# Kernel optimization log

Measured on AMD Instinct MI355X. Metric: run time of the kernel, lower is better.

Reference implementation:

```python
import jax, jax.numpy as jnp
import numpy as np

T, B, H, EMB, EVO, A = 700, 32, 800, 32, 21, 60
DIN = EMB + EVO            # 53 = embedding + evolutionary profile
RNN_OUT = 2 * H + DIN      # 1653 = bi-LSTM output + skip connection

BOND_LENGTHS = jnp.array([145.801, 152.326, 132.868], jnp.float32)
BOND_ANGLES = jnp.array([2.124, 1.941, 2.028], jnp.float32)
INIT_MAT = jnp.array([[-np.sqrt(0.5), np.sqrt(1.5), 0.0],
                      [-np.sqrt(2.0), 0.0, 0.0],
                      [0.0, 0.0, 0.0]], jnp.float32)


def setup_inputs():
    key = jax.random.key(0)
    ks = jax.random.split(key, 12)
    s = 0.03  # ~ pytorch LSTM uniform(-1/sqrt(H), 1/sqrt(H)) scale

    def lstm_params(k, d):
        k1, k2, k3 = jax.random.split(k, 3)
        return (jax.random.normal(k1, (4 * H, d)) * s,
                jax.random.normal(k2, (4 * H, H)) * s,
                jax.random.normal(k3, (4 * H,)) * s)  # b = b_ih + b_hh fused

    Wih0f, Whh0f, b0f = lstm_params(ks[0], DIN)
    Wih0b, Whh0b, b0b = lstm_params(ks[1], DIN)
    Wih1f, Whh1f, b1f = lstm_params(ks[2], 2 * H)
    Wih1b, Whh1b, b1b = lstm_params(ks[3], 2 * H)
    emb = jax.random.normal(ks[4], (21, EMB)) * s
    emb = emb.at[0].set(0.0)  # padding_idx=0
    fcW = jax.random.normal(ks[5], (A, RNN_OUT)) * s
    fcb = jax.random.normal(ks[6], (A,)) * s
    alphabet = jnp.pi * jnp.tanh(jax.random.normal(ks[7], (A, 3)))  # angularize
    primary = jax.random.randint(ks[8], (T, B), 0, 21)
    evolutionary = jax.random.normal(ks[9], (T, B, EVO))
    return {"primary": primary, "evolutionary": evolutionary, "seq_length": T,
            "emb": emb,
            "Wih0f": Wih0f, "Whh0f": Whh0f, "b0f": b0f,
            "Wih0b": Wih0b, "Whh0b": Whh0b, "b0b": b0b,
            "Wih1f": Wih1f, "Whh1f": Whh1f, "b1f": b1f,
            "Wih1b": Wih1b, "Whh1b": Whh1b, "b1b": b1b,
            "fcW": fcW, "fcb": fcb, "alphabet": alphabet}


def lstm_dir(xs, Wih, Whh, b, reverse):
    """One direction of an LSTM over xs [T, B, D] -> [T, B, H] (PyTorch gate order i,f,g,o)."""
    if reverse:
        xs = xs[::-1]
    xg = jnp.einsum('tbd,gd->tbg', xs, Wih) + b  # precompute input projection

    def step(carry, g_t):
        h, c = carry
        g = g_t + h @ Whh.T
        i, f, gg, o = jnp.split(g, 4, axis=-1)
        c = jax.nn.sigmoid(f) * c + jax.nn.sigmoid(i) * jnp.tanh(gg)
        h = jax.nn.sigmoid(o) * jnp.tanh(c)
        return (h, c), h

    z = jnp.zeros((xs.shape[1], Whh.shape[1]), xs.dtype)
    _, hs = jax.lax.scan(step, (z, z), xg)
    return hs[::-1] if reverse else hs


def dihedral_to_point(dih):
    """dih [T, B, 3] -> backbone points in local frames [3T, B, 3]."""
    rct = BOND_LENGTHS * jnp.cos(jnp.pi - BOND_ANGLES)
    rst = BOND_LENGTHS * jnp.sin(jnp.pi - BOND_ANGLES)
    px = jnp.broadcast_to(rct, dih.shape)
    pts = jnp.stack([px, jnp.cos(dih) * rst, jnp.sin(dih) * rst], axis=-1)  # [T,B,3,3]
    t, b = dih.shape[0], dih.shape[1]
    return pts.transpose(0, 2, 1, 3).reshape(3 * t, b, 3)


def point_to_coordinate(pts):
    """Sequential NeRF extension: pts [3T, B, 3] -> coords [3T, B, 3]."""
    b_sz = pts.shape[1]
    a = jnp.broadcast_to(INIT_MAT[0], (b_sz, 3))
    b = jnp.broadcast_to(INIT_MAT[1], (b_sz, 3))
    c = jnp.broadcast_to(INIT_MAT[2], (b_sz, 3))

    def norm(v):
        return v / jnp.sqrt(jnp.sum(v * v, axis=-1, keepdims=True) + 1e-12)

    def step(carry, p):
        a, b, c = carry
        bc = norm(c - b)
        n = norm(jnp.cross(b - a, bc))
        coord = c + p[:, 0:1] * bc + p[:, 1:2] * jnp.cross(n, bc) + p[:, 2:3] * n
        return (b, c, coord), coord

    _, coords = jax.lax.scan(step, (a, b, c), pts)
    return coords


def reference(primary, evolutionary, seq_length, emb,
              Wih0f, Whh0f, b0f, Wih0b, Whh0b, b0b,
              Wih1f, Whh1f, b1f, Wih1b, Whh1b, b1b,
              fcW, fcb, alphabet):
    # seq_length == T for all sequences, so packing is identity.
    x = jnp.concatenate([emb[primary], evolutionary], axis=-1)  # [T,B,53]
    h0 = jnp.concatenate([lstm_dir(x, Wih0f, Whh0f, b0f, False),
                          lstm_dir(x, Wih0b, Whh0b, b0b, True)], axis=-1)   # [T,B,1600]
    h1 = jnp.concatenate([lstm_dir(h0, Wih1f, Whh1f, b1f, False),
                          lstm_dir(h0, Wih1b, Whh1b, b1b, True)], axis=-1)  # [T,B,1600]
    out = jnp.concatenate([h1, x], axis=-1)  # skip connection -> [T,B,1653]
    logits = jnp.einsum('tbd,ad->tba', out, fcW) + fcb  # [T,B,60]
    probs = jax.nn.softmax(logits, axis=-1)  # alphabet_temperature = 1.0
    dih = jnp.arctan2(probs @ jnp.sin(alphabet), probs @ jnp.cos(alphabet))  # [T,B,3]
    return point_to_coordinate(dihedral_to_point(dih))  # [3T, B, 3]
```

## Files before the change

### kernel.cpp

```cpp
#include <hip/hip_runtime.h>
#include <hip/hip_bf16.h>
#include <math.h>


typedef unsigned int u32;
typedef unsigned long long u64;
typedef __bf16 bf16x8 __attribute__((ext_vector_type(8)));
typedef float  f32x4  __attribute__((ext_vector_type(4)));

#define TT 700
#define BT 32
#define HROW 1664
#define CH 50
#define NCH (TT / CH)
#define SLOT ((size_t)2 * CH * 3200 * 32)
#define LDS_L0 (108 * 512 + 102400)
#define LDS_L1 (100 * 512 + 102400)

__device__ __forceinline__ f32x4 mfma16(bf16x8 a, bf16x8 b, f32x4 c) {
  return __builtin_amdgcn_mfma_f32_16x16x32_bf16(a, b, c, 0, 0, 0);
}
__device__ __forceinline__ float sigf(float x) { return 1.f / (1.f + __expf(-x)); }

#define ALOAD(p)    __hip_atomic_load((p), __ATOMIC_RELAXED, __HIP_MEMORY_SCOPE_AGENT)
#define ASTORE(p,v) __hip_atomic_store((p), (v), __ATOMIC_RELAXED, __HIP_MEMORY_SCOPE_AGENT)

__device__ __forceinline__ void lds_barrier() {
  asm volatile("s_waitcnt lgkmcnt(0)" ::: "memory");
  __builtin_amdgcn_s_barrier();
}

__device__ __forceinline__ bf16x8 cvt8(f32x4 a, f32x4 b) {
  bf16x8 r;
  r[0] = (__bf16)a[0]; r[1] = (__bf16)a[1]; r[2] = (__bf16)a[2]; r[3] = (__bf16)a[3];
  r[4] = (__bf16)b[0]; r[5] = (__bf16)b[1]; r[6] = (__bf16)b[2]; r[7] = (__bf16)b[3];
  return r;
}

#define QUAD_TRANSPOSE(l_, a0, a1, a2, a3, o0, o1, o2, o3)                   \
  {                                                                          \
    float s0 = __shfl_xor(a0, 1), s1 = __shfl_xor(a1, 1);                    \
    float s2 = __shfl_xor(a2, 1), s3 = __shfl_xor(a3, 1);                    \
    const bool e1 = ((l_) & 1) == 0;                                         \
    float n0 = e1 ? a0 : s1, n1 = e1 ? s0 : a1;                              \
    float n2 = e1 ? a2 : s3, n3 = e1 ? s2 : a3;                              \
    float t0 = __shfl_xor(n0, 2), t1 = __shfl_xor(n1, 2);                    \
    float t2 = __shfl_xor(n2, 2), t3 = __shfl_xor(n3, 2);                    \
    const bool e2 = ((l_) & 2) == 0;                                         \
    o0 = e2 ? n0 : t2; o1 = e2 ? n1 : t3;                                    \
    o2 = e2 ? t0 : n2; o3 = e2 ? t1 : n3;                                    \
  }

__global__ void pack_wx0_kernel(const float* Wih0f, const float* Wih0b, __bf16* wx0) {
  int idx = blockIdx.x * 256 + threadIdx.x;
  if (idx >= 2 * 3200 * 64) return;
  int d = idx / (3200 * 64);
  int r = (idx / 64) % 3200;
  int k = idx % 64;
  const float* W = d ? Wih0b : Wih0f;
  wx0[idx] = (k < 53) ? (__bf16)W[(size_t)r * 53 + k] : (__bf16)0.f;
}

__global__ void pack_fc_kernel(const float* fcW, __bf16* wfc) {
  int idx = blockIdx.x * 256 + threadIdx.x;
  if (idx >= 64 * 1664) return;
  int a = idx / 1664, k = idx % 1664;
  __bf16 v = (__bf16)0.f;
  if (a < 60 && k < 1653) v = (__bf16)fcW[(size_t)a * 1653 + k];
  wfc[idx] = v;
}

__global__ void xpad_kernel(const int* primary, const float* evo,
                            const float* emb, __bf16* xpad) {
  int idx = blockIdx.x * 256 + threadIdx.x;
  int t = idx >> 11;
  int b = (idx >> 6) & 31;
  int k = idx & 63;
  __bf16 v = (__bf16)0.f;
  if (k < 32)      v = (__bf16)emb[primary[t * 32 + b] * 32 + k];
  else if (k < 53) v = (__bf16)evo[((size_t)t * 32 + b) * 21 + (k - 32)];
  xpad[idx] = v;
}

__global__ void small_init_kernel(__bf16* zerobuf, u32* flags,
                                  float* sinA, float* cosA, const float* alpha) {
  int idx = blockIdx.x * 256 + threadIdx.x;
  if (idx < 32 * HROW) zerobuf[idx] = (__bf16)0.f;
  if (idx < 11392) flags[idx] = 0u;
  int j = idx - 32 * HROW;
  if (j >= 0 && j < 192) {
    if (j < 180) {
      float v = alpha[j];
      sinA[j] = sinf(v);
      cosA[j] = cosf(v);
    } else { sinA[j] = 0.f; cosA[j] = 0.f; }
  }
}

__device__ __forceinline__ void wait_lines(u32* flags, int base, int count,
                                           unsigned gen) {
  const int tid = threadIdx.x;
  if (tid < 64) {
    int spin = 0;
    for (;;) {
      bool ok = true;
      for (int j = tid; j < count; j += 64)
        ok = ok && (ALOAD(flags + (size_t)(base + j) * 32) >= gen);
      if (__popcll(__ballot(ok)) == 64) break;
      if (++spin > 24) __builtin_amdgcn_s_sleep(1);
    }
  }
  __syncthreads();
}

__device__ __forceinline__ void rec_barrier(u32* flags, unsigned gen,
                                            int base, int count) {
  asm volatile("s_waitcnt vmcnt(0)" ::: "memory");
  __syncthreads();
  if (threadIdx.x == 0) ASTORE(flags + (size_t)blockIdx.x * 32, gen);
  wait_lines(flags, base, count, gen);
}

struct L0Args {
  const __bf16 *xpad, *wx0, *zero;
  const float *Whh0f, *Whh0b, *b0f, *b0b;
  __bf16* h0;
  u32* flags;
};

__global__ __launch_bounds__(256, 1) void lstm_l0(L0Args A) {
  extern __shared__ __bf16 u2[];
  const int wg = blockIdx.x, d = wg / 50, u0 = (wg % 50) * 16;
  const int tid = threadIdx.x, w = tid >> 6, l = tid & 63;
  const int nidx = l & 15, q = l >> 4, bL = l & 31, gl = l >> 5;
  const int dcol = d * 832;
  const int row = (nidx & 3) * 800 + u0 + 4 * w + (nidx >> 2);
  const float bias_n = (d ? A.b0b : A.b0f)[row];
  const float* wrf = (d ? A.Whh0b : A.Whh0f) + (size_t)row * 800 + q * 8;
  __bf16* wlds = u2 + 108 * 256;

#pragma unroll
  for (int sl = 0; sl < 25; ++sl) {
    f32x4 wa = *(const f32x4*)(wrf + sl * 32);
    f32x4 wb = *(const f32x4*)(wrf + sl * 32 + 4);
    *(bf16x8*)(wlds + ((size_t)(w * 25 + sl) * 64 + l) * 8) = cvt8(wa, wb);
  }
  const __bf16* wx_row = A.wx0 + (size_t)d * 3200 * 64 + (size_t)row * 64 + q * 8;
  bf16x8 wx_r0 = *(const bf16x8*)wx_row;
  bf16x8 wx_r1 = *(const bf16x8*)(wx_row + 32);
  __syncthreads();

  float cA = 0.f, cB = 0.f;
#pragma unroll 1
  for (int s = 0; s < TT; ++s) {
    const int tt = d ? (TT - 1 - s) : s;
    const __bf16* hprev =
        (s == 0) ? A.zero : (A.h0 + (size_t)(d ? tt + 1 : tt - 1) * (BT * HROW));

    bf16x8 hreg[13];
    const __bf16* hsrc = hprev + (size_t)bL * HROW + dcol;
#pragma unroll
    for (int i = 0; i < 12; ++i)
      hreg[i] = *(const bf16x8*)(hsrc + (i * 8 + w * 2 + gl) * 8);
    if (w < 2) hreg[12] = *(const bf16x8*)(hsrc + (96 + w * 2 + gl) * 8);
    bf16x8 xv = *(const bf16x8*)(A.xpad + ((size_t)tt * BT + bL) * 64 + (tid >> 5) * 8);

#pragma unroll
    for (int i = 0; i < 12; ++i)
      *(bf16x8*)(u2 + (size_t)(i * 8 + w * 2 + gl) * 256 + bL * 8) = hreg[i];
    if (w < 2)
      *(bf16x8*)(u2 + (size_t)(96 + w * 2 + gl) * 256 + bL * 8) = hreg[12];
    *(bf16x8*)(u2 + (size_t)(100 + (tid >> 5)) * 256 + bL * 8) = xv;
    __syncthreads();

    f32x4 acc0 = {0.f, 0.f, 0.f, 0.f}, acc1 = {0.f, 0.f, 0.f, 0.f};
#pragma unroll
    for (int sl = 0; sl < 27; ++sl) {
      bf16x8 bfr;
      if (sl < 25)
        bfr = *(const bf16x8*)(wlds + ((size_t)(w * 25 + sl) * 64 + l) * 8);
      else
        bfr = (sl == 25) ? wx_r0 : wx_r1;
      const __bf16* ab = u2 + (size_t)(sl * 4 + q) * 256 + nidx * 8;
      bf16x8 a0 = *(const bf16x8*)ab;
      bf16x8 a1 = *(const bf16x8*)(ab + 128);
      acc0 = mfma16(a0, bfr, acc0);
      acc1 = mfma16(a1, bfr, acc1);
    }

    {
      float a0 = acc0[0] + bias_n, a1 = acc0[1] + bias_n,
            a2 = acc0[2] + bias_n, a3 = acc0[3] + bias_n;
      float e0 = acc1[0] + bias_n, e1v = acc1[1] + bias_n,
            e2v = acc1[2] + bias_n, e3 = acc1[3] + bias_n;
      float iA, fA, gA, oA, iB, fB, gB, oB;
      QUAD_TRANSPOSE(l, a0, a1, a2, a3, iA, fA, gA, oA);
      QUAD_TRANSPOSE(l, e0, e1v, e2v, e3, iB, fB, gB, oB);
      cA = sigf(fA) * cA + sigf(iA) * tanhf(gA);
      float hA = sigf(oA) * tanhf(cA);
      cB = sigf(fB) * cB + sigf(iB) * tanhf(gB);
      float hB = sigf(oB) * tanhf(cB);
      float hA2 = __shfl_xor(hA, 4);
      float hB2 = __shfl_xor(hB, 4);
      if ((l & 4) == 0) {
        const int bA = q * 4 + (nidx & 3);
        const int colp = dcol + u0 + 4 * w + (nidx >> 2);
        union { u32 u; __bf16 h2[2]; } pk;
        pk.h2[0] = (__bf16)hA; pk.h2[1] = (__bf16)hA2;
        ASTORE((u32*)(A.h0 + ((size_t)tt * BT + bA) * HROW + colp), pk.u);
        pk.h2[0] = (__bf16)hB; pk.h2[1] = (__bf16)hB2;
        ASTORE((u32*)(A.h0 + ((size_t)tt * BT + bA + 16) * HROW + colp), pk.u);
      }
    }

    if (s < TT - 1) rec_barrier(A.flags, (unsigned)(s + 1), d * 50, 50);
  }
}

struct L1Args {
  const __bf16 *h0, *zero;
  const float *Whh1f, *Whh1b, *Wih1f, *Wih1b, *b1f, *b1b;
  __bf16 *h1, *xg;
  u32* flags;
};

__global__ __launch_bounds__(256, 1) void lstm_l1(L1Args A) {
  extern __shared__ __bf16 u2[];
  const int tid = threadIdx.x, w = tid >> 6, l = tid & 63;
  const int nidx = l & 15, q = l >> 4, bL = l & 31, gl = l >> 5;
  __bf16* wlds = u2 + 100 * 256;

  if (blockIdx.x < 100) {
    const int wg = blockIdx.x, d = wg / 50, u0 = (wg % 50) * 16;
    const int dcol = d * 832;
    const int row = (nidx & 3) * 800 + u0 + 4 * w + (nidx >> 2);
    {
      const float* wrf = (d ? A.Whh1b : A.Whh1f) + (size_t)row * 800 + q * 8;
#pragma unroll
      for (int sl = 0; sl < 25; ++sl) {
        f32x4 wa = *(const f32x4*)(wrf + sl * 32);
        f32x4 wb = *(const f32x4*)(wrf + sl * 32 + 4);
        *(bf16x8*)(wlds + ((size_t)(w * 25 + sl) * 64 + l) * 8) = cvt8(wa, wb);
      }
    }
    __syncthreads();
    float cA = 0.f, cB = 0.f;

    for (int k = 0; k < NCH; ++k) {
      wait_lines(A.flags, 100, 156, (unsigned)(k + 1));
      const __bf16* buf = A.xg + (size_t)(k & 1) * SLOT;
      const u64* xga0 = (const u64*)(buf + ((size_t)(d * CH) * 3200 + row) * 32 + q * 4);
      u64 x0 = ALOAD(xga0);
      u64 x1 = ALOAD(xga0 + 4);
#pragma unroll 1
      for (int si = 0; si < CH; ++si) {
        const int s = k * CH + si;
        const int tt = d ? (TT - 1 - s) : s;
        const __bf16* hprev =
            (s == 0) ? A.zero
                     : (A.h1 + (size_t)(d ? tt + 1 : tt - 1) * (BT * HROW));

        u64 cx0 = x0, cx1 = x1;
        if (si + 1 < CH) {
          const u64* xgn = (const u64*)(buf +
              ((size_t)(d * CH + si + 1) * 3200 + row) * 32 + q * 4);
          x0 = ALOAD(xgn);
          x1 = ALOAD(xgn + 4);
        }

        bf16x8 hreg[13];
        const __bf16* hsrc = hprev + (size_t)bL * HROW + dcol;
#pragma unroll
        for (int i = 0; i < 12; ++i)
          hreg[i] = *(const bf16x8*)(hsrc + (i * 8 + w * 2 + gl) * 8);
        if (w < 2) hreg[12] = *(const bf16x8*)(hsrc + (96 + w * 2 + gl) * 8);

        union { u64 u; __bf16 h[4]; } ux0, ux1;
        ux0.u = cx0; ux1.u = cx1;
        f32x4 acc0 = {(float)ux0.h[0], (float)ux0.h[1],
                      (float)ux0.h[2], (float)ux0.h[3]};
        f32x4 acc1 = {(float)ux1.h[0], (float)ux1.h[1],
                      (float)ux1.h[2], (float)ux1.h[3]};

#pragma unroll
        for (int i = 0; i < 12; ++i)
          *(bf16x8*)(u2 + (size_t)(i * 8 + w * 2 + gl) * 256 + bL * 8) = hreg[i];
        if (w < 2)
          *(bf16x8*)(u2 + (size_t)(96 + w * 2 + gl) * 256 + bL * 8) = hreg[12];
        lds_barrier();

#pragma unroll
        for (int sl = 0; sl < 25; ++sl) {
          bf16x8 bfr = *(const bf16x8*)(wlds + ((size_t)(w * 25 + sl) * 64 + l) * 8);
          const __bf16* ab = u2 + (size_t)(sl * 4 + q) * 256 + nidx * 8;
          bf16x8 a0 = *(const bf16x8*)ab;
          bf16x8 a1 = *(const bf16x8*)(ab + 128);
          acc0 = mfma16(a0, bfr, acc0);
          acc1 = mfma16(a1, bfr, acc1);
        }

        {
          float a0 = acc0[0], a1 = acc0[1], a2 = acc0[2], a3 = acc0[3];
          float e0 = acc1[0], e1v = acc1[1], e2v = acc1[2], e3 = acc1[3];
          float iA, fA, gA, oA, iB, fB, gB, oB;
          QUAD_TRANSPOSE(l, a0, a1, a2, a3, iA, fA, gA, oA);
          QUAD_TRANSPOSE(l, e0, e1v, e2v, e3, iB, fB, gB, oB);
          cA = sigf(fA) * cA + sigf(iA) * tanhf(gA);
          float hA = sigf(oA) * tanhf(cA);
          cB = sigf(fB) * cB + sigf(iB) * tanhf(gB);
          float hB = sigf(oB) * tanhf(cB);
          float hA2 = __shfl_xor(hA, 4);
          float hB2 = __shfl_xor(hB, 4);
          if ((l & 4) == 0) {
            const int bA = q * 4 + (nidx & 3);
            const int colp = dcol + u0 + 4 * w + (nidx >> 2);
            union { u32 u; __bf16 h2[2]; } pk;
            pk.h2[0] = (__bf16)hA; pk.h2[1] = (__bf16)hA2;
            ASTORE((u32*)(A.h1 + ((size_t)tt * BT + bA) * HROW + colp), pk.u);
            pk.h2[0] = (__bf16)hB; pk.h2[1] = (__bf16)hB2;
            ASTORE((u32*)(A.h1 + ((size_t)tt * BT + bA + 16) * HROW + colp), pk.u);
          }
        }

        if (s < TT - 1) rec_barrier(A.flags, (unsigned)(s + 1), 0 + d * 50, 50);
      }
    }
  } else {
    const int g = blockIdx.x - 100;
    const int u_begin = (g * 400) / 156;
    const int u_end   = ((g + 1) * 400) / 156;
    const int nslots  = (u_end - u_begin) * 50;
    const int rh = w >> 1, bh = w & 1;

    bf16x8 pre[13];
    f32x4 acc = {0.f, 0.f, 0.f, 0.f};
    int cur_tl = -1;
    float bn = 0.f;
    int rr = 0;

    for (int k = 0; k < NCH; ++k) {
      if (k >= 2) wait_lines(A.flags, 0, 100, (unsigned)((k - 1) * CH));
      __bf16* buf = A.xg + (size_t)(k & 1) * SLOT;

      {
        const int th0 = u_begin & 1;
        const int dir0 = (u_begin >> 1) / 100;
        const int tloc0 = th0 * 25;
        const int t0 = dir0 ? (TT - 1 - k * CH - tloc0) : (k * CH + tloc0);
        const __bf16* hs = A.h0 + ((size_t)t0 * BT + bL) * HROW;
#pragma unroll
        for (int i = 0; i < 12; ++i)
          pre[i] = *(const bf16x8*)(hs + (i * 8 + w * 2 + gl) * 8);
        if (w < 2) pre[12] = *(const bf16x8*)(hs + (96 + w * 2 + gl) * 8);
      }

#pragma unroll 1
      for (int s = 0; s < nslots; ++s) {
        const int u = u_begin + s / 50;
        const int r = s % 50;
        const int tl = u >> 1, th = u & 1;
        const int tloc = th * 25 + (r >> 1);
        const int pass = r & 1;
        const int dir = tl / 100, rt = tl % 100;
        const int rbase = rt * 32;

        if (tl != cur_tl) {
          cur_tl = tl;
          const float* W = dir ? A.Wih1b : A.Wih1f;
          __syncthreads();
          for (int i = w * 25; i < w * 25 + 25; ++i) {
            const int rhh = i / 50, sl = i % 50;
            const int rrr = rbase + rhh * 16 + nidx;
            const float* wp = W + (size_t)rrr * 1600 + sl * 32 + q * 8;
            f32x4 wa = *(const f32x4*)wp;
            f32x4 wb = *(const f32x4*)(wp + 4);
            *(bf16x8*)(wlds + ((size_t)i * 64 + l) * 8) = cvt8(wa, wb);
          }
          __syncthreads();
          rr = rbase + rh * 16 + nidx;
          bn = (dir ? A.b1b : A.b1f)[rr];
        }

#pragma unroll
        for (int i = 0; i < 12; ++i)
          *(bf16x8*)(u2 + (size_t)(i * 8 + w * 2 + gl) * 256 + bL * 8) = pre[i];
        if (w < 2)
          *(bf16x8*)(u2 + (size_t)(96 + w * 2 + gl) * 256 + bL * 8) = pre[12];
        lds_barrier();

        if (s + 1 < nslots) {
          const int s2 = s + 1;
          const int un = u_begin + s2 / 50;
          const int r2 = s2 % 50;
          const int thn = un & 1;
          const int tlocn = thn * 25 + (r2 >> 1);
          const int passn = r2 & 1;
          const int dirn = (un >> 1) / 100;
          const int tn = dirn ? (TT - 1 - k * CH - tlocn) : (k * CH + tlocn);
          const __bf16* hs = A.h0 + ((size_t)tn * BT + bL) * HROW + passn * 832;
#pragma unroll
          for (int i = 0; i < 12; ++i)
            pre[i] = *(const bf16x8*)(hs + (i * 8 + w * 2 + gl) * 8);
          if (w < 2) pre[12] = *(const bf16x8*)(hs + (96 + w * 2 + gl) * 8);
        }
        __builtin_amdgcn_sched_barrier(0);

        if (pass == 0) acc = f32x4{0.f, 0.f, 0.f, 0.f};
#pragma unroll
        for (int sl = 0; sl < 25; ++sl) {
          bf16x8 b = *(const bf16x8*)(wlds +
              ((size_t)(rh * 50 + pass * 25 + sl) * 64 + l) * 8);
          bf16x8 a = *(const bf16x8*)(u2 +
              (size_t)(sl * 4 + q) * 256 + (bh * 16 + nidx) * 8);
          acc = mfma16(a, b, acc);
        }
        lds_barrier();

        if (pass == 1) {
          union { u64 u; __bf16 h[4]; } pv;
#pragma unroll
          for (int r2 = 0; r2 < 4; ++r2) pv.h[r2] = (__bf16)(acc[r2] + bn);
          ASTORE((u64*)(buf + ((size_t)(dir * CH + tloc) * 3200 + rr) * 32 +
                        bh * 16 + q * 4), pv.u);
        }
      }
      asm volatile("s_waitcnt vmcnt(0)" ::: "memory");
      __syncthreads();
      if (tid == 0) ASTORE(A.flags + (size_t)(100 + g) * 32, (unsigned)(k + 1));
    }
  }
}

__global__ __launch_bounds__(256) void fc_kernel(
    const __bf16* __restrict__ h1, const __bf16* __restrict__ xpad,
    const __bf16* __restrict__ wfc, const float* __restrict__ fcb,
    const float* __restrict__ sinA, const float* __restrict__ cosA,
    float* __restrict__ pts) {
  __shared__ float lg[32 * 64];
  const int t = blockIdx.x, tid = threadIdx.x;
  const int wave = tid >> 6, lane = tid & 63, nidx = lane & 15, q = lane >> 4;
  const int a_col = wave * 16 + nidx;
  const __bf16* wrow = wfc + (size_t)a_col * 1664 + q * 8;
  const __bf16* h1row = h1 + (size_t)t * BT * HROW;
  const __bf16* xrow  = xpad + (size_t)t * BT * 64;
  f32x4 acc0 = {0.f, 0.f, 0.f, 0.f}, acc1 = {0.f, 0.f, 0.f, 0.f};
#pragma unroll
  for (int sl = 0; sl < 52; ++sl) {
    const int k = sl * 32 + q * 8;
    bf16x8 a0, a1;
    if (sl < 50) {
      const int kp = (sl < 25) ? k : (k + 32);
      a0 = *(const bf16x8*)(h1row + (size_t)nidx * HROW + kp);
      a1 = *(const bf16x8*)(h1row + (size_t)(16 + nidx) * HROW + kp);
    } else {
      a0 = *(const bf16x8*)(xrow + nidx * 64 + (k - 1600));
      a1 = *(const bf16x8*)(xrow + (16 + nidx) * 64 + (k - 1600));
    }
    bf16x8 bfr = *(const bf16x8*)(wrow + sl * 32);
    acc0 = mfma16(a0, bfr, acc0);
    acc1 = mfma16(a1, bfr, acc1);
  }
  const float bn = (a_col < 60) ? fcb[a_col] : -1e30f;
#pragma unroll
  for (int r = 0; r < 4; ++r) {
    lg[(q * 4 + r) * 64 + a_col]      = acc0[r] + bn;
    lg[(16 + q * 4 + r) * 64 + a_col] = acc1[r] + bn;
  }
  __syncthreads();

  const int b = tid >> 3, j = tid & 7;
  float v[8];
  float m = -1e30f;
#pragma unroll
  for (int k2 = 0; k2 < 8; ++k2) {
    v[k2] = lg[b * 64 + j + 8 * k2];
    m = fmaxf(m, v[k2]);
  }
  m = fmaxf(m, __shfl_xor(m, 1, 8));
  m = fmaxf(m, __shfl_xor(m, 2, 8));
  m = fmaxf(m, __shfl_xor(m, 4, 8));
  float s = 0.f;
#pragma unroll
  for (int k2 = 0; k2 < 8; ++k2) { v[k2] = __expf(v[k2] - m); s += v[k2]; }
  s += __shfl_xor(s, 1, 8);
  s += __shfl_xor(s, 2, 8);
  s += __shfl_xor(s, 4, 8);
  const float inv = 1.f / s;
  float ps[3] = {0.f, 0.f, 0.f}, pc[3] = {0.f, 0.f, 0.f};
#pragma unroll
  for (int k2 = 0; k2 < 8; ++k2) {
    const int a = j + 8 * k2;
    const float p = v[k2] * inv;
#pragma unroll
    for (int c = 0; c < 3; ++c) {
      ps[c] += p * sinA[a * 3 + c];
      pc[c] += p * cosA[a * 3 + c];
    }
  }
#pragma unroll
  for (int c = 0; c < 3; ++c) {
    ps[c] += __shfl_xor(ps[c], 1, 8);
    ps[c] += __shfl_xor(ps[c], 2, 8);
    ps[c] += __shfl_xor(ps[c], 4, 8);
    pc[c] += __shfl_xor(pc[c], 1, 8);
    pc[c] += __shfl_xor(pc[c], 2, 8);
    pc[c] += __shfl_xor(pc[c], 4, 8);
  }
  if (j == 0) {
    const float BL[3] = {145.801f, 152.326f, 132.868f};
    const float BA[3] = {2.124f, 1.941f, 2.028f};
#pragma unroll
    for (int c = 0; c < 3; ++c) {
      const float ang = 3.14159265358979323846f - BA[c];
      const float rct = BL[c] * cosf(ang), rst = BL[c] * sinf(ang);
      const float dih = atan2f(ps[c], pc[c]);
      float* o = pts + ((size_t)(3 * t + c) * BT + b) * 3;
      o[0] = rct;
      o[1] = cosf(dih) * rst;
      o[2] = sinf(dih) * rst;
    }
  }
}

__global__ void nerf_kernel(const float* __restrict__ pts, float* __restrict__ out) {
  const int b = threadIdx.x;
  if (b >= 32) return;
  float ax = -0.70710678f, ay = 1.22474487f, az = 0.f;
  float bx = -1.41421356f, by = 0.f, bz = 0.f;
  float cx = 0.f, cy = 0.f, cz = 0.f;
#pragma unroll 4
  for (int i = 0; i < 3 * TT; ++i) {
    const float* p = pts + ((size_t)i * BT + b) * 3;
    const float p0 = p[0], p1 = p[1], p2 = p[2];
    float ux = cx - bx, uy = cy - by, uz = cz - bz;
    const float ri = rsqrtf(ux * ux + uy * uy + uz * uz + 1e-12f);
    ux *= ri; uy *= ri; uz *= ri;
    const float wx = bx - ax, wy = by - ay, wz = bz - az;
    float nx = wy * uz - wz * uy, ny = wz * ux - wx * uz, nz = wx * uy - wy * ux;
    const float rn = rsqrtf(nx * nx + ny * ny + nz * nz + 1e-12f);
    nx *= rn; ny *= rn; nz *= rn;
    const float mx = ny * uz - nz * uy, my = nz * ux - nx * uz, mz = nx * uy - ny * ux;
    const float ox = cx + p0 * ux + p1 * mx + p2 * nx;
    const float oy = cy + p0 * uy + p1 * my + p2 * ny;
    const float oz = cz + p0 * uz + p1 * mz + p2 * nz;
    out[((size_t)i * BT + b) * 3 + 0] = ox;
    out[((size_t)i * BT + b) * 3 + 1] = oy;
    out[((size_t)i * BT + b) * 3 + 2] = oz;
    ax = bx; ay = by; az = bz;
    bx = cx; by = cy; bz = cz;
    cx = ox; cy = oy; cz = oz;
  }
}

extern "C" void kernel_launch(void* const* d_in, const int* in_sizes, int n_in,
                              void* d_out, int out_size, void* d_ws, size_t ws_size,
                              hipStream_t stream) {
  (void)in_sizes; (void)n_in; (void)out_size;
  const int*   primary = (const int*)d_in[0];
  const float* evo     = (const float*)d_in[1];
  const float* emb     = (const float*)d_in[3];
  const float* Wih0f   = (const float*)d_in[4];
  const float* Whh0f   = (const float*)d_in[5];
  const float* b0f     = (const float*)d_in[6];
  const float* Wih0b   = (const float*)d_in[7];
  const float* Whh0b   = (const float*)d_in[8];
  const float* b0b     = (const float*)d_in[9];
  const float* Wih1f   = (const float*)d_in[10];
  const float* Whh1f   = (const float*)d_in[11];
  const float* b1f     = (const float*)d_in[12];
  const float* Wih1b   = (const float*)d_in[13];
  const float* Whh1b   = (const float*)d_in[14];
  const float* b1b     = (const float*)d_in[15];
  const float* fcW     = (const float*)d_in[16];
  const float* fcb     = (const float*)d_in[17];
  const float* alpha   = (const float*)d_in[18];

  char* ws = (char*)d_ws;
  size_t off = 0;
  auto take = [&](size_t n) -> void* {
    void* p = ws + off;
    off += (n + 511) & ~(size_t)511;
    return p;
  };
  __bf16* xpad = (__bf16*)take((size_t)TT * BT * 64 * 2);
  __bf16* zb   = (__bf16*)take((size_t)BT * HROW * 2);
  __bf16* wx0  = (__bf16*)take((size_t)2 * 3200 * 64 * 2);
  __bf16* wfc  = (__bf16*)take((size_t)64 * 1664 * 2);
  float*  sinA = (float*)take(192 * 4);
  float*  cosA = (float*)take(192 * 4);
  float*  pts  = (float*)take((size_t)3 * TT * BT * 3 * 4);
  u32*    flags0 = (u32*)take(11392 * 4);
  u32*    flags1 = flags0 + 3200;
  __bf16* xg   = (__bf16*)take(2 * SLOT * 2);
  __bf16* h0   = (__bf16*)take((size_t)TT * BT * HROW * 2);
  __bf16* h1   = (__bf16*)take((size_t)TT * BT * HROW * 2);
  if (off > ws_size) return;

  static int lds_cfg = 0;
  if (!lds_cfg) {
    hipFuncSetAttribute((const void*)lstm_l0,
                        hipFuncAttributeMaxDynamicSharedMemorySize, LDS_L0);
    hipFuncSetAttribute((const void*)lstm_l1,
                        hipFuncAttributeMaxDynamicSharedMemorySize, LDS_L1);
    lds_cfg = 1;
  }

  pack_wx0_kernel<<<1600, 256, 0, stream>>>(Wih0f, Wih0b, wx0);
  pack_fc_kernel<<<(64 * 1664 + 255) / 256, 256, 0, stream>>>(fcW, wfc);
  xpad_kernel<<<(TT * BT * 64) / 256, 256, 0, stream>>>(primary, evo, emb, xpad);
  small_init_kernel<<<209, 256, 0, stream>>>(zb, flags0, sinA, cosA, alpha);

  L0Args a0;
  a0.xpad = xpad; a0.wx0 = wx0; a0.zero = zb;
  a0.Whh0f = Whh0f; a0.Whh0b = Whh0b; a0.b0f = b0f; a0.b0b = b0b;
  a0.h0 = h0; a0.flags = flags0;
  lstm_l0<<<100, 256, LDS_L0, stream>>>(a0);

  L1Args a1;
  a1.h0 = h0; a1.zero = zb;
  a1.Whh1f = Whh1f; a1.Whh1b = Whh1b;
  a1.Wih1f = Wih1f; a1.Wih1b = Wih1b;
  a1.b1f = b1f; a1.b1b = b1b;
  a1.h1 = h1; a1.xg = xg; a1.flags = flags1;
  lstm_l1<<<256, 256, LDS_L1, stream>>>(a1);

  fc_kernel<<<TT, 256, 0, stream>>>(h1, xpad, wfc, fcb, sinA, cosA, pts);
  nerf_kernel<<<1, 64, 0, stream>>>(pts, (float*)d_out);
}
```

Before: 9.200 ms.

## Fuse both LSTM layers into one persistent kernel overlapping layer-1 input projection

Merges the layer-0 and layer-1 recurrent kernels into a single persistent launch. Recurrent blocks run layer 0 and then layer 1, while the 156 helper blocks compute layer-1 input projections chunk by chunk as soon as the needed layer-0 timesteps from both directions are ready. The helpers follow a reordered chunk schedule with six xg buffer slots, so layer-1 can start on its first chunks without waiting for all of layer 0. This is meant to hide the input-projection GEMM and the launch gap behind the layer-0 recurrence. It costs more workspace and adds complex flag-based cross-block dependencies, falling back to two slots in sequential order if the workspace is too small.

```diff
diff --git a/kernel.cpp b/kernel.cpp
--- a/kernel.cpp
+++ b/kernel.cpp
@@ -14,8 +14,7 @@
 #define CH 50
 #define NCH (TT / CH)
 #define SLOT ((size_t)2 * CH * 3200 * 32)
-#define LDS_L0 (108 * 512 + 102400)
-#define LDS_L1 (100 * 512 + 102400)
+#define LDS_FU (108 * 512 + 102400)
 
 __device__ __forceinline__ f32x4 mfma16(bf16x8 a, bf16x8 b, f32x4 c) {
   return __builtin_amdgcn_mfma_f32_16x16x32_bf16(a, b, c, 0, 0, 0);
@@ -121,152 +120,46 @@
   wait_lines(flags, base, count, gen);
 }
 
-struct L0Args {
+struct FusedArgs {
   const __bf16 *xpad, *wx0, *zero;
   const float *Whh0f, *Whh0b, *b0f, *b0b;
-  __bf16* h0;
-  u32* flags;
+  const float *Whh1f, *Whh1b, *Wih1f, *Wih1b, *b1f, *b1b;
+  __bf16 *h0, *h1, *xg;
+  u32 *f0, *f1;
+  int mode;
 };
 
-__global__ __launch_bounds__(256, 1) void lstm_l0(L0Args A) {
-  extern __shared__ __bf16 u2[];
-  const int wg = blockIdx.x, d = wg / 50, u0 = (wg % 50) * 16;
-  const int tid = threadIdx.x, w = tid >> 6, l = tid & 63;
-  const int nidx = l & 15, q = l >> 4, bL = l & 31, gl = l >> 5;
-  const int dcol = d * 832;
-  const int row = (nidx & 3) * 800 + u0 + 4 * w + (nidx >> 2);
-  const float bias_n = (d ? A.b0b : A.b0f)[row];
-  const float* wrf = (d ? A.Whh0b : A.Whh0f) + (size_t)row * 800 + q * 8;
-  __bf16* wlds = u2 + 108 * 256;
-
-#pragma unroll
-  for (int sl = 0; sl < 25; ++sl) {
-    f32x4 wa = *(const f32x4*)(wrf + sl * 32);
-    f32x4 wb = *(const f32x4*)(wrf + sl * 32 + 4);
-    *(bf16x8*)(wlds + ((size_t)(w * 25 + sl) * 64 + l) * 8) = cvt8(wa, wb);
-  }
-  const __bf16* wx_row = A.wx0 + (size_t)d * 3200 * 64 + (size_t)row * 64 + q * 8;
-  bf16x8 wx_r0 = *(const bf16x8*)wx_row;
-  bf16x8 wx_r1 = *(const bf16x8*)(wx_row + 32);
-  __syncthreads();
-
-  float cA = 0.f, cB = 0.f;
-#pragma unroll 1
-  for (int s = 0; s < TT; ++s) {
-    const int tt = d ? (TT - 1 - s) : s;
-    const __bf16* hprev =
-        (s == 0) ? A.zero : (A.h0 + (size_t)(d ? tt + 1 : tt - 1) * (BT * HROW));
-
-    bf16x8 hreg[13];
-    const __bf16* hsrc = hprev + (size_t)bL * HROW + dcol;
-#pragma unroll
-    for (int i = 0; i < 12; ++i)
-      hreg[i] = *(const bf16x8*)(hsrc + (i * 8 + w * 2 + gl) * 8);
-    if (w < 2) hreg[12] = *(const bf16x8*)(hsrc + (96 + w * 2 + gl) * 8);
-    bf16x8 xv = *(const bf16x8*)(A.xpad + ((size_t)tt * BT + bL) * 64 + (tid >> 5) * 8);
-
-#pragma unroll
-    for (int i = 0; i < 12; ++i)
-      *(bf16x8*)(u2 + (size_t)(i * 8 + w * 2 + gl) * 256 + bL * 8) = hreg[i];
-    if (w < 2)
-      *(bf16x8*)(u2 + (size_t)(96 + w * 2 + gl) * 256 + bL * 8) = hreg[12];
-    *(bf16x8*)(u2 + (size_t)(100 + (tid >> 5)) * 256 + bL * 8) = xv;
-    __syncthreads();
-
-    f32x4 acc0 = {0.f, 0.f, 0.f, 0.f}, acc1 = {0.f, 0.f, 0.f, 0.f};
-#pragma unroll
-    for (int sl = 0; sl < 27; ++sl) {
-      bf16x8 bfr;
-      if (sl < 25)
-        bfr = *(const bf16x8*)(wlds + ((size_t)(w * 25 + sl) * 64 + l) * 8);
-      else
-        bfr = (sl == 25) ? wx_r0 : wx_r1;
-      const __bf16* ab = u2 + (size_t)(sl * 4 + q) * 256 + nidx * 8;
-      bf16x8 a0 = *(const bf16x8*)ab;
-      bf16x8 a1 = *(const bf16x8*)(ab + 128);
-      acc0 = mfma16(a0, bfr, acc0);
-      acc1 = mfma16(a1, bfr, acc1);
-    }
-
-    {
-      float a0 = acc0[0] + bias_n, a1 = acc0[1] + bias_n,
-            a2 = acc0[2] + bias_n, a3 = acc0[3] + bias_n;
-      float e0 = acc1[0] + bias_n, e1v = acc1[1] + bias_n,
-            e2v = acc1[2] + bias_n, e3 = acc1[3] + bias_n;
-      float iA, fA, gA, oA, iB, fB, gB, oB;
-      QUAD_TRANSPOSE(l, a0, a1, a2, a3, iA, fA, gA, oA);
-      QUAD_TRANSPOSE(l, e0, e1v, e2v, e3, iB, fB, gB, oB);
-      cA = sigf(fA) * cA + sigf(iA) * tanhf(gA);
-      float hA = sigf(oA) * tanhf(cA);
-      cB = sigf(fB) * cB + sigf(iB) * tanhf(gB);
-      float hB = sigf(oB) * tanhf(cB);
-      float hA2 = __shfl_xor(hA, 4);
-      float hB2 = __shfl_xor(hB, 4);
-      if ((l & 4) == 0) {
-        const int bA = q * 4 + (nidx & 3);
-        const int colp = dcol + u0 + 4 * w + (nidx >> 2);
-        union { u32 u; __bf16 h2[2]; } pk;
-        pk.h2[0] = (__bf16)hA; pk.h2[1] = (__bf16)hA2;
-        ASTORE((u32*)(A.h0 + ((size_t)tt * BT + bA) * HROW + colp), pk.u);
-        pk.h2[0] = (__bf16)hB; pk.h2[1] = (__bf16)hB2;
-        ASTORE((u32*)(A.h0 + ((size_t)tt * BT + bA + 16) * HROW + colp), pk.u);
-      }
-    }
-
-    if (s < TT - 1) rec_barrier(A.flags, (unsigned)(s + 1), d * 50, 50);
-  }
-}
-
-struct L1Args {
-  const __bf16 *h0, *zero;
-  const float *Whh1f, *Whh1b, *Wih1f, *Wih1b, *b1f, *b1b;
-  __bf16 *h1, *xg;
-  u32* flags;
-};
-
-__global__ __launch_bounds__(256, 1) void lstm_l1(L1Args A) {
+__global__ __launch_bounds__(256, 1) void lstm_fused(FusedArgs A) {
   extern __shared__ __bf16 u2[];
   const int tid = threadIdx.x, w = tid >> 6, l = tid & 63;
   const int nidx = l & 15, q = l >> 4, bL = l & 31, gl = l >> 5;
-  __bf16* wlds = u2 + 100 * 256;
+  __bf16* wlds = u2 + 108 * 256;
 
   if (blockIdx.x < 100) {
     const int wg = blockIdx.x, d = wg / 50, u0 = (wg % 50) * 16;
     const int dcol = d * 832;
     const int row = (nidx & 3) * 800 + u0 + 4 * w + (nidx >> 2);
+
     {
-      const float* wrf = (d ? A.Whh1b : A.Whh1f) + (size_t)row * 800 + q * 8;
+      const float bias_n = (d ? A.b0b : A.b0f)[row];
+      const float* wrf = (d ? A.Whh0b : A.Whh0f) + (size_t)row * 800 + q * 8;
 #pragma unroll
       for (int sl = 0; sl < 25; ++sl) {
         f32x4 wa = *(const f32x4*)(wrf + sl * 32);
         f32x4 wb = *(const f32x4*)(wrf + sl * 32 + 4);
         *(bf16x8*)(wlds + ((size_t)(w * 25 + sl) * 64 + l) * 8) = cvt8(wa, wb);
       }
-    }
-    __syncthreads();
-    float cA = 0.f, cB = 0.f;
-
-    for (int k = 0; k < NCH; ++k) {
-      wait_lines(A.flags, 100, 156, (unsigned)(k + 1));
-      const __bf16* buf = A.xg + (size_t)(k & 1) * SLOT;
-      const u64* xga0 = (const u64*)(buf + ((size_t)(d * CH) * 3200 + row) * 32 + q * 4);
-      u64 x0 = ALOAD(xga0);
-      u64 x1 = ALOAD(xga0 + 4);
+      const __bf16* wx_row = A.wx0 + (size_t)d * 3200 * 64 + (size_t)row * 64 + q * 8;
+      bf16x8 wx_r0 = *(const bf16x8*)wx_row;
+      bf16x8 wx_r1 = *(const bf16x8*)(wx_row + 32);
+      __syncthreads();
+
+      float cA = 0.f, cB = 0.f;
 #pragma unroll 1
-      for (int si = 0; si < CH; ++si) {
-        const int s = k * CH + si;
+      for (int s = 0; s < TT; ++s) {
         const int tt = d ? (TT - 1 - s) : s;
         const __bf16* hprev =
-            (s == 0) ? A.zero
-                     : (A.h1 + (size_t)(d ? tt + 1 : tt - 1) * (BT * HROW));
-
-        u64 cx0 = x0, cx1 = x1;
-        if (si + 1 < CH) {
-          const u64* xgn = (const u64*)(buf +
-              ((size_t)(d * CH + si + 1) * 3200 + row) * 32 + q * 4);
-          x0 = ALOAD(xgn);
-          x1 = ALOAD(xgn + 4);
-        }
+            (s == 0) ? A.zero : (A.h0 + (size_t)(d ? tt + 1 : tt - 1) * (BT * HROW));
 
         bf16x8 hreg[13];
         const __bf16* hsrc = hprev + (size_t)bL * HROW + dcol;
@@ -274,24 +167,24 @@
         for (int i = 0; i < 12; ++i)
           hreg[i] = *(const bf16x8*)(hsrc + (i * 8 + w * 2 + gl) * 8);
         if (w < 2) hreg[12] = *(const bf16x8*)(hsrc + (96 + w * 2 + gl) * 8);
-
-        union { u64 u; __bf16 h[4]; } ux0, ux1;
-        ux0.u = cx0; ux1.u = cx1;
-        f32x4 acc0 = {(float)ux0.h[0], (float)ux0.h[1],
-                      (float)ux0.h[2], (float)ux0.h[3]};
-        f32x4 acc1 = {(float)ux1.h[0], (float)ux1.h[1],
-                      (float)ux1.h[2], (float)ux1.h[3]};
+        bf16x8 xv = *(const bf16x8*)(A.xpad + ((size_t)tt * BT + bL) * 64 + (tid >> 5) * 8);
 
 #pragma unroll
         for (int i = 0; i < 12; ++i)
           *(bf16x8*)(u2 + (size_t)(i * 8 + w * 2 + gl) * 256 + bL * 8) = hreg[i];
         if (w < 2)
           *(bf16x8*)(u2 + (size_t)(96 + w * 2 + gl) * 256 + bL * 8) = hreg[12];
-        lds_barrier();
-
-#pragma unroll
-        for (int sl = 0; sl < 25; ++sl) {
-          bf16x8 bfr = *(const bf16x8*)(wlds + ((size_t)(w * 25 + sl) * 64 + l) * 8);
+        *(bf16x8*)(u2 + (size_t)(100 + (tid >> 5)) * 256 + bL * 8) = xv;
+        __syncthreads();
+
+        f32x4 acc0 = {0.f, 0.f, 0.f, 0.f}, acc1 = {0.f, 0.f, 0.f, 0.f};
+#pragma unroll
+        for (int sl = 0; sl < 27; ++sl) {
+          bf16x8 bfr;
+          if (sl < 25)
+            bfr = *(const bf16x8*)(wlds + ((size_t)(w * 25 + sl) * 64 + l) * 8);
+          else
+            bfr = (sl == 25) ? wx_r0 : wx_r1;
           const __bf16* ab = u2 + (size_t)(sl * 4 + q) * 256 + nidx * 8;
           bf16x8 a0 = *(const bf16x8*)ab;
           bf16x8 a1 = *(const bf16x8*)(ab + 128);
@@ -300,8 +193,10 @@
         }
 
         {
-          float a0 = acc0[0], a1 = acc0[1], a2 = acc0[2], a3 = acc0[3];
-          float e0 = acc1[0], e1v = acc1[1], e2v = acc1[2], e3 = acc1[3];
+          float a0 = acc0[0] + bias_n, a1 = acc0[1] + bias_n,
+                a2 = acc0[2] + bias_n, a3 = acc0[3] + bias_n;
+          float e0 = acc1[0] + bias_n, e1v = acc1[1] + bias_n,
+                e2v = acc1[2] + bias_n, e3 = acc1[3] + bias_n;
           float iA, fA, gA, oA, iB, fB, gB, oB;
           QUAD_TRANSPOSE(l, a0, a1, a2, a3, iA, fA, gA, oA);
           QUAD_TRANSPOSE(l, e0, e1v, e2v, e3, iB, fB, gB, oB);
@@ -316,16 +211,120 @@
             const int colp = dcol + u0 + 4 * w + (nidx >> 2);
             union { u32 u; __bf16 h2[2]; } pk;
             pk.h2[0] = (__bf16)hA; pk.h2[1] = (__bf16)hA2;
-            ASTORE((u32*)(A.h1 + ((size_t)tt * BT + bA) * HROW + colp), pk.u);
+            ASTORE((u32*)(A.h0 + ((size_t)tt * BT + bA) * HROW + colp), pk.u);
             pk.h2[0] = (__bf16)hB; pk.h2[1] = (__bf16)hB2;
-            ASTORE((u32*)(A.h1 + ((size_t)tt * BT + bA + 16) * HROW + colp), pk.u);
+            ASTORE((u32*)(A.h0 + ((size_t)tt * BT + bA + 16) * HROW + colp), pk.u);
           }
         }
 
-        if (s < TT - 1) rec_barrier(A.flags, (unsigned)(s + 1), 0 + d * 50, 50);
+        if (s < TT - 1) rec_barrier(A.f0, (unsigned)(s + 1), d * 50, 50);
+      }
+
+      asm volatile("s_waitcnt vmcnt(0)" ::: "memory");
+      __syncthreads();
+      if (tid == 0) ASTORE(A.f0 + (size_t)wg * 32, (unsigned)TT);
+    }
+
+    {
+      const int POS1[14]  = {4, 5, 6, 7, 8, 2, 0, 1, 3, 9, 10, 11, 12, 13};
+      const int SLOT1[14] = {4, 5, 4, 5, 4, 2, 0, 1, 3, 5, 0, 1, 2, 3};
+      const float* wrf = (d ? A.Whh1b : A.Whh1f) + (size_t)row * 800 + q * 8;
+      __syncthreads();
+#pragma unroll
+      for (int sl = 0; sl < 25; ++sl) {
+        f32x4 wa = *(const f32x4*)(wrf + sl * 32);
+        f32x4 wb = *(const f32x4*)(wrf + sl * 32 + 4);
+        *(bf16x8*)(wlds + ((size_t)(w * 25 + sl) * 64 + l) * 8) = cvt8(wa, wb);
+      }
+      __syncthreads();
+      float cA = 0.f, cB = 0.f;
+
+      for (int k = 0; k < NCH; ++k) {
+        const int pos = A.mode ? POS1[k] : k;
+        wait_lines(A.f1, 100, 156, (unsigned)(pos + 1));
+        const int slot = A.mode ? SLOT1[k] : (k & 1);
+        const __bf16* buf = A.xg + (size_t)slot * SLOT;
+        const u64* xga0 = (const u64*)(buf + ((size_t)(d * CH) * 3200 + row) * 32 + q * 4);
+        u64 x0 = ALOAD(xga0);
+        u64 x1 = ALOAD(xga0 + 4);
+#pragma unroll 1
+        for (int si = 0; si < CH; ++si) {
+          const int s = k * CH + si;
+          const int tt = d ? (TT - 1 - s) : s;
+          const __bf16* hprev =
+              (s == 0) ? A.zero
+                       : (A.h1 + (size_t)(d ? tt + 1 : tt - 1) * (BT * HROW));
+
+          u64 cx0 = x0, cx1 = x1;
+          if (si + 1 < CH) {
+            const u64* xgn = (const u64*)(buf +
+                ((size_t)(d * CH + si + 1) * 3200 + row) * 32 + q * 4);
+            x0 = ALOAD(xgn);
+            x1 = ALOAD(xgn + 4);
+          }
+
+          bf16x8 hreg[13];
+          const __bf16* hsrc = hprev + (size_t)bL * HROW + dcol;
+#pragma unroll
+          for (int i = 0; i < 12; ++i)
+            hreg[i] = *(const bf16x8*)(hsrc + (i * 8 + w * 2 + gl) * 8);
+          if (w < 2) hreg[12] = *(const bf16x8*)(hsrc + (96 + w * 2 + gl) * 8);
+
+          union { u64 u; __bf16 h[4]; } ux0, ux1;
+          ux0.u = cx0; ux1.u = cx1;
+          f32x4 acc0 = {(float)ux0.h[0], (float)ux0.h[1],
+                        (float)ux0.h[2], (float)ux0.h[3]};
+          f32x4 acc1 = {(float)ux1.h[0], (float)ux1.h[1],
+                        (float)ux1.h[2], (float)ux1.h[3]};
+
+#pragma unroll
+          for (int i = 0; i < 12; ++i)
+            *(bf16x8*)(u2 + (size_t)(i * 8 + w * 2 + gl) * 256 + bL * 8) = hreg[i];
+          if (w < 2)
+            *(bf16x8*)(u2 + (size_t)(96 + w * 2 + gl) * 256 + bL * 8) = hreg[12];
+          lds_barrier();
+
+#pragma unroll
+          for (int sl = 0; sl < 25; ++sl) {
+            bf16x8 bfr = *(const bf16x8*)(wlds + ((size_t)(w * 25 + sl) * 64 + l) * 8);
+            const __bf16* ab = u2 + (size_t)(sl * 4 + q) * 256 + nidx * 8;
+            bf16x8 a0 = *(const bf16x8*)ab;
+            bf16x8 a1 = *(const bf16x8*)(ab + 128);
+            acc0 = mfma16(a0, bfr, acc0);
+            acc1 = mfma16(a1, bfr, acc1);
+          }
+
+          {
+            float a0 = acc0[0], a1 = acc0[1], a2 = acc0[2], a3 = acc0[3];
+            float e0 = acc1[0], e1v = acc1[1], e2v = acc1[2], e3 = acc1[3];
+            float iA, fA, gA, oA, iB, fB, gB, oB;
+            QUAD_TRANSPOSE(l, a0, a1, a2, a3, iA, fA, gA, oA);
+            QUAD_TRANSPOSE(l, e0, e1v, e2v, e3, iB, fB, gB, oB);
+            cA = sigf(fA) * cA + sigf(iA) * tanhf(gA);
+            float hA = sigf(oA) * tanhf(cA);
+            cB = sigf(fB) * cB + sigf(iB) * tanhf(gB);
+            float hB = sigf(oB) * tanhf(cB);
+            float hA2 = __shfl_xor(hA, 4);
+            float hB2 = __shfl_xor(hB, 4);
+            if ((l & 4) == 0) {
+              const int bA = q * 4 + (nidx & 3);
+              const int colp = dcol + u0 + 4 * w + (nidx >> 2);
+              union { u32 u; __bf16 h2[2]; } pk;
+              pk.h2[0] = (__bf16)hA; pk.h2[1] = (__bf16)hA2;
+              ASTORE((u32*)(A.h1 + ((size_t)tt * BT + bA) * HROW + colp), pk.u);
+              pk.h2[0] = (__bf16)hB; pk.h2[1] = (__bf16)hB2;
+              ASTORE((u32*)(A.h1 + ((size_t)tt * BT + bA + 16) * HROW + colp), pk.u);
+            }
+          }
+
+          if (s < TT - 1) rec_barrier(A.f1, (unsigned)(s + 1), 0 + d * 50, 50);
+        }
       }
     }
   } else {
+    const int P1[14]    = {6, 7, 5, 8, 0, 1, 2, 3, 4, 9, 10, 11, 12, 13};
+    const int WAIT1[14] = {-1,-1,-1,-1,-1,-1, 0, 1, 2, 3, 6, 7, 5, 8};
+    const int SLOT1[14] = {4, 5, 4, 5, 4, 2, 0, 1, 3, 5, 0, 1, 2, 3};
     const int g = blockIdx.x - 100;
     const int u_begin = (g * 400) / 156;
     const int u_end   = ((g + 1) * 400) / 156;
@@ -338,9 +337,15 @@
     float bn = 0.f;
     int rr = 0;
 
-    for (int k = 0; k < NCH; ++k) {
-      if (k >= 2) wait_lines(A.flags, 0, 100, (unsigned)((k - 1) * CH));
-      __bf16* buf = A.xg + (size_t)(k & 1) * SLOT;
+    for (int ki = 0; ki < NCH; ++ki) {
+      const int k = A.mode ? P1[ki] : ki;
+      {
+        const int n1 = (k + 1) * CH, n2 = TT - k * CH;
+        wait_lines(A.f0, 0, 100, (unsigned)(n1 > n2 ? n1 : n2));
+      }
+      const int wc = A.mode ? WAIT1[ki] : (ki - 2);
+      if (wc >= 0) wait_lines(A.f1, 0, 100, (unsigned)((wc + 1) * CH));
+      __bf16* buf = A.xg + (size_t)(A.mode ? SLOT1[k] : (k & 1)) * SLOT;
 
       {
         const int th0 = u_begin & 1;
@@ -426,7 +431,7 @@
       }
       asm volatile("s_waitcnt vmcnt(0)" ::: "memory");
       __syncthreads();
-      if (tid == 0) ASTORE(A.flags + (size_t)(100 + g) * 32, (unsigned)(k + 1));
+      if (tid == 0) ASTORE(A.f1 + (size_t)(100 + g) * 32, (unsigned)(ki + 1));
     }
   }
 }
@@ -575,6 +580,16 @@
   const float* fcb     = (const float*)d_in[17];
   const float* alpha   = (const float*)d_in[18];
 
+  auto al = [](size_t n) { return (n + 511) & ~(size_t)511; };
+  const size_t slotB = SLOT * 2;
+  const size_t fixedB =
+      al((size_t)TT * BT * 64 * 2) + al((size_t)BT * HROW * 2) +
+      al((size_t)2 * 3200 * 64 * 2) + al((size_t)64 * 1664 * 2) +
+      al(192 * 4) + al(192 * 4) + al((size_t)3 * TT * BT * 3 * 4) +
+      al(11392 * 4) + 2 * al((size_t)TT * BT * HROW * 2);
+  int slots = 6, mode = 1;
+  if (fixedB + al((size_t)6 * slotB) > ws_size) { slots = 2; mode = 0; }
+
   char* ws = (char*)d_ws;
   size_t off = 0;
   auto take = [&](size_t n) -> void* {
@@ -591,17 +606,15 @@
   float*  pts  = (float*)take((size_t)3 * TT * BT * 3 * 4);
   u32*    flags0 = (u32*)take(11392 * 4);
   u32*    flags1 = flags0 + 3200;
-  __bf16* xg   = (__bf16*)take(2 * SLOT * 2);
+  __bf16* xg   = (__bf16*)take((size_t)slots * slotB);
   __bf16* h0   = (__bf16*)take((size_t)TT * BT * HROW * 2);
   __bf16* h1   = (__bf16*)take((size_t)TT * BT * HROW * 2);
   if (off > ws_size) return;
 
   static int lds_cfg = 0;
   if (!lds_cfg) {
-    hipFuncSetAttribute((const void*)lstm_l0,
-                        hipFuncAttributeMaxDynamicSharedMemorySize, LDS_L0);
-    hipFuncSetAttribute((const void*)lstm_l1,
-                        hipFuncAttributeMaxDynamicSharedMemorySize, LDS_L1);
+    hipFuncSetAttribute((const void*)lstm_fused,
+                        hipFuncAttributeMaxDynamicSharedMemorySize, LDS_FU);
     lds_cfg = 1;
   }
 
@@ -610,19 +623,16 @@
   xpad_kernel<<<(TT * BT * 64) / 256, 256, 0, stream>>>(primary, evo, emb, xpad);
   small_init_kernel<<<209, 256, 0, stream>>>(zb, flags0, sinA, cosA, alpha);
 
-  L0Args a0;
-  a0.xpad = xpad; a0.wx0 = wx0; a0.zero = zb;
-  a0.Whh0f = Whh0f; a0.Whh0b = Whh0b; a0.b0f = b0f; a0.b0b = b0b;
-  a0.h0 = h0; a0.flags = flags0;
-  lstm_l0<<<100, 256, LDS_L0, stream>>>(a0);
-
-  L1Args a1;
-  a1.h0 = h0; a1.zero = zb;
-  a1.Whh1f = Whh1f; a1.Whh1b = Whh1b;
-  a1.Wih1f = Wih1f; a1.Wih1b = Wih1b;
-  a1.b1f = b1f; a1.b1b = b1b;
-  a1.h1 = h1; a1.xg = xg; a1.flags = flags1;
-  lstm_l1<<<256, 256, LDS_L1, stream>>>(a1);
+  FusedArgs fa;
+  fa.xpad = xpad; fa.wx0 = wx0; fa.zero = zb;
+  fa.Whh0f = Whh0f; fa.Whh0b = Whh0b; fa.b0f = b0f; fa.b0b = b0b;
+  fa.Whh1f = Whh1f; fa.Whh1b = Whh1b;
+  fa.Wih1f = Wih1f; fa.Wih1b = Wih1b;
+  fa.b1f = b1f; fa.b1b = b1b;
+  fa.h0 = h0; fa.h1 = h1; fa.xg = xg;
+  fa.f0 = flags0; fa.f1 = flags1;
+  fa.mode = mode;
+  lstm_fused<<<256, 256, LDS_FU, stream>>>(fa);
 
   fc_kernel<<<TT, 256, 0, stream>>>(h1, xpad, wfc, fcb, sinA, cosA, pts);
   nerf_kernel<<<1, 64, 0, stream>>>(pts, (float*)d_out);
```

Result: no change. 9.062 ms (-1.5%).
